# Kernel tuning notes

Measured on AMD Instinct MI355X. Metric: run time of the kernel, lower is better.

## Reference

```python
import jax, jax.numpy as jnp
import numpy as np

NEG_INF = -9e15  # matches the torch module's zero_vec constant
ALPHA = 0.2      # LeakyReLU negative slope


def setup_inputs() -> dict:
    key = jax.random.key(0)
    k1, k2, k3, k4, k5, k6 = jax.random.split(key, 6)
    N_t, N_o, F_in, F_out = 8192, 8192, 256, 64
    return {
        "t_input": jax.random.normal(k1, (N_t, F_in), dtype=jnp.float32),
        "o_input": jax.random.normal(k2, (N_o, F_in), dtype=jnp.float32),
        "W_t": jax.random.normal(k3, (F_in, F_out), dtype=jnp.float32) * 0.1,
        "W_o": jax.random.normal(k4, (F_in, F_out), dtype=jnp.float32) * 0.1,
        "a": jax.random.normal(k5, (2 * F_out, 1), dtype=jnp.float32) * 0.1,
        "adj": jax.random.randint(k6, (N_t, N_o), 0, 2, dtype=jnp.int32),
    }


def reference(t_input, o_input, W_t, W_o, a, adj):
    # Linear projections
    h_t = t_input @ W_t            # [N_t, F]
    h_o = o_input @ W_o            # [N_o, F]
    F_out = h_t.shape[1]
    a_t = a[:F_out, 0]             # [F]
    a_o = a[F_out:, 0]             # [F]
    # e[i,j] = leakyrelu(cat(h_t[i], h_o[j]) . a) = leakyrelu(h_t[i].a_t + h_o[j].a_o)
    # (avoids materializing the N_t*N_o*2F concat tensor; same math)
    e = jax.nn.leaky_relu(
        (h_t @ a_t)[:, None] + (h_o @ a_o)[None, :], negative_slope=ALPHA
    )                              # [N_t, N_o]
    attention = jnp.where(adj > 0, e, NEG_INF)
    attention = jax.nn.softmax(attention, axis=1)
    # dropout is identity at eval time
    h_prime = attention @ h_o      # [N_t, F]
    return jax.nn.elu(h_prime)     # concat=True
```

## Files before the change

### kernel.cpp

```cpp
#include <hip/hip_runtime.h>
#include <math.h>

#define NT 8192
#define NO 8192
#define FIN 256
#define FOUT 64
#define SPLIT 8
#define JSP (NO/SPLIT)
#define ROWT 64

#define OFF_ST  ((size_t)0)
#define OFF_SO  (OFF_ST + (size_t)NT)
#define OFF_WT  (OFF_SO + (size_t)NO)
#define OFF_WO  (OFF_WT + (size_t)FIN)
#define OFF_NUM (OFF_WO + (size_t)FIN)
#define OFF_DEN (OFF_NUM + (size_t)SPLIT*NT*FOUT)
#define OFF_HOB (OFF_DEN + (size_t)SPLIT*NT)
#define OFF_ETA (OFF_HOB + (size_t)NO*FOUT/2)

typedef __attribute__((ext_vector_type(8))) short short8;
typedef __attribute__((ext_vector_type(4))) float float4v;

static __device__ __forceinline__ unsigned short f2bf(float x) {
  unsigned int u = __float_as_uint(x);
  unsigned int r = (u + 0x7fffu + ((u >> 16) & 1u)) >> 16;
  return (unsigned short)r;
}
static __device__ __forceinline__ int pk2(float a, float b) {
  return (int)((unsigned int)f2bf(a) | ((unsigned int)f2bf(b) << 16));
}
static __device__ __forceinline__ float bflo(int p) {
  return __uint_as_float(((unsigned int)p) << 16);
}
static __device__ __forceinline__ float bfhi(int p) {
  return __uint_as_float(((unsigned int)p) & 0xffff0000u);
}

__global__ void k_wvec(const float* __restrict__ Wt, const float* __restrict__ Wo,
                       const float* __restrict__ a, float* __restrict__ ws) {
  int k = threadIdx.x;
  float s1 = 0.f, s2 = 0.f;
#pragma unroll
  for (int fq = 0; fq < FOUT/4; ++fq) {
    float4 wt4 = *(const float4*)(Wt + (size_t)k*FOUT + fq*4);
    float4 wo4 = *(const float4*)(Wo + (size_t)k*FOUT + fq*4);
    float4 at4 = *(const float4*)(a + fq*4);
    float4 ao4 = *(const float4*)(a + FOUT + fq*4);
    s1 += wt4.x*at4.x + wt4.y*at4.y + wt4.z*at4.z + wt4.w*at4.w;
    s2 += wo4.x*ao4.x + wo4.y*ao4.y + wo4.z*ao4.z + wo4.w*ao4.w;
  }
  ws[OFF_WT + k] = s1;
  ws[OFF_WO + k] = s2;
}

__global__ void k_st(const float* __restrict__ tin, float* __restrict__ ws) {
  int lane = threadIdx.x & 63;
  int wv   = threadIdx.x >> 6;
  int row  = blockIdx.x * 4 + wv;
  float4 v = ((const float4*)(tin + (size_t)row*FIN))[lane];
  float4 w = ((const float4*)(ws + OFF_WT))[lane];
  float p = v.x*w.x + v.y*w.y + v.z*w.z + v.w*w.w;
#pragma unroll
  for (int m = 32; m >= 1; m >>= 1) p += __shfl_xor(p, m, 64);
  if (lane == 0) ws[OFF_ST + row] = p;
}

__global__ void k_ho(const float* __restrict__ oin, const float* __restrict__ Wo,
                     const float* __restrict__ a, float* __restrict__ ws) {
  unsigned short* hobp = (unsigned short*)(ws + OFF_HOB);
  int lane = threadIdx.x & 63;
  int wv = __builtin_amdgcn_readfirstlane(threadIdx.x >> 6);
  int r0 = blockIdx.x * 16 + wv * 4;
  const float* ob = oin + (size_t)r0 * FIN;
  float acc[4];
#pragma unroll
  for (int r = 0; r < 4; ++r) acc[r] = 0.f;
#pragma unroll 2
  for (int k = 0; k < FIN; k += 4) {
    float w0 = Wo[(size_t)(k+0)*FOUT + lane];
    float w1 = Wo[(size_t)(k+1)*FOUT + lane];
    float w2 = Wo[(size_t)(k+2)*FOUT + lane];
    float w3 = Wo[(size_t)(k+3)*FOUT + lane];
#pragma unroll
    for (int r = 0; r < 4; ++r) {
      float4 ov = *(const float4*)(ob + (size_t)r*FIN + k);
      acc[r] = fmaf(ov.x, w0, acc[r]);
      acc[r] = fmaf(ov.y, w1, acc[r]);
      acc[r] = fmaf(ov.z, w2, acc[r]);
      acc[r] = fmaf(ov.w, w3, acc[r]);
    }
  }
  float ao = a[FOUT + lane];
  int fg = lane >> 4, n16 = lane & 15;
#pragma unroll
  for (int r = 0; r < 4; ++r) {
    int j = r0 + r;
    int jt = j >> 5, jl = j & 31;
    int ldst = (jl >> 3) * 16 + n16;
    int e = jl & 7;
    hobp[(((size_t)jt*4 + fg)*64 + ldst)*8 + e] = f2bf(acc[r]);
    float p = acc[r] * ao;
#pragma unroll
    for (int m = 32; m >= 1; m >>= 1) p += __shfl_xor(p, m, 64);
    if (lane == 0) ws[OFF_SO + j] = p;
  }
}

__global__ void k_etab(float* __restrict__ ws) {
  int j = blockIdx.x * 256 + threadIdx.x;
  float s = ws[OFF_SO + j];
  ws[OFF_ETA + 2*j + 0] = __expf(s);
  ws[OFF_ETA + 2*j + 1] = __expf(0.2f * s);
}

__launch_bounds__(256, 4)
__global__ void k_attn(const int* __restrict__ adj, float* __restrict__ ws) {
  const float* st = ws + OFF_ST;
  const float* etab = ws + OFF_ETA;
  const unsigned short* hobp = (const unsigned short*)(ws + OFF_HOB);
  float* gnum = ws + OFF_NUM;
  float* gden = ws + OFF_DEN;

  int t = threadIdx.x;
  int wv = t >> 6, lane = t & 63;
  int bx = blockIdx.x;
  int s  = bx & (SPLIT - 1);
  int bi = bx >> 3;
  int i0 = bi * ROWT;
  int jb = s * JSP;

  int rsrc = lane >> 2, csrc = lane & 3;
  int irow_s = i0 + wv*16 + rsrc;
  float sti  = st[irow_s];
  float esti  = __expf(sti);
  float esti2 = __expf(0.2f * sti);
  float ethr  = __expf(-sti);

  const int* arow = adj + (size_t)irow_s * NO + jb + csrc*8;
  const float* ep = etab + (size_t)(jb + csrc*8) * 2;
  const unsigned short* hpb = hobp + (size_t)(jb >> 5) * 2048 + lane*8;

  int r16 = lane & 15, kg = lane >> 4;
  int sidx4 = ((r16 * 4 + kg) << 2);

  float4v acc0 = (float4v)0.f, acc1 = (float4v)0.f;
  float4v acc2 = (float4v)0.f, acc3 = (float4v)0.f;
  float dsum = 0.f;

  int4 a0 = *(const int4*)(arow);
  int4 a1 = *(const int4*)(arow + 4);

#pragma unroll 1
  for (int tt = 0; tt < JSP/32; ++tt) {
    int ttn = (tt < JSP/32 - 1) ? tt + 1 : tt;
    int4 n0 = *(const int4*)(arow + ttn*32);
    int4 n1 = *(const int4*)(arow + ttn*32 + 4);

    const float* e_ = ep + tt*64;
    float4 e0 = *(const float4*)(e_);
    float4 e1 = *(const float4*)(e_ + 4);
    float4 e2 = *(const float4*)(e_ + 8);
    float4 e3 = *(const float4*)(e_ + 12);
    const unsigned short* hb = hpb + (size_t)tt*2048;
    short8 b0 = *(const short8*)(hb);
    short8 b1 = *(const short8*)(hb + 512);
    short8 b2 = *(const short8*)(hb + 1024);
    short8 b3 = *(const short8*)(hb + 1536);

    float w0 = ((e0.x >= ethr) ? esti*e0.x : esti2*e0.y); w0 = (a0.x > 0) ? w0 : 0.f;
    float w1 = ((e0.z >= ethr) ? esti*e0.z : esti2*e0.w); w1 = (a0.y > 0) ? w1 : 0.f;
    float w2 = ((e1.x >= ethr) ? esti*e1.x : esti2*e1.y); w2 = (a0.z > 0) ? w2 : 0.f;
    float w3 = ((e1.z >= ethr) ? esti*e1.z : esti2*e1.w); w3 = (a0.w > 0) ? w3 : 0.f;
    float w4 = ((e2.x >= ethr) ? esti*e2.x : esti2*e2.y); w4 = (a1.x > 0) ? w4 : 0.f;
    float w5 = ((e2.z >= ethr) ? esti*e2.z : esti2*e2.w); w5 = (a1.y > 0) ? w5 : 0.f;
    float w6 = ((e3.x >= ethr) ? esti*e3.x : esti2*e3.y); w6 = (a1.z > 0) ? w6 : 0.f;
    float w7 = ((e3.z >= ethr) ? esti*e3.z : esti2*e3.w); w7 = (a1.w > 0) ? w7 : 0.f;

    int p0 = pk2(w0, w1);
    int p1 = pk2(w2, w3);
    int p2 = pk2(w4, w5);
    int p3 = pk2(w6, w7);
    dsum += bflo(p0) + bfhi(p0) + bflo(p1) + bfhi(p1)
          + bflo(p2) + bfhi(p2) + bflo(p3) + bfhi(p3);

    int4 ai;
    ai.x = __builtin_amdgcn_ds_bpermute(sidx4, p0);
    ai.y = __builtin_amdgcn_ds_bpermute(sidx4, p1);
    ai.z = __builtin_amdgcn_ds_bpermute(sidx4, p2);
    ai.w = __builtin_amdgcn_ds_bpermute(sidx4, p3);
    short8 afrag = *(short8*)&ai;

    acc0 = __builtin_amdgcn_mfma_f32_16x16x32_bf16(afrag, b0, acc0, 0, 0, 0);
    acc1 = __builtin_amdgcn_mfma_f32_16x16x32_bf16(afrag, b1, acc1, 0, 0, 0);
    acc2 = __builtin_amdgcn_mfma_f32_16x16x32_bf16(afrag, b2, acc2, 0, 0, 0);
    acc3 = __builtin_amdgcn_mfma_f32_16x16x32_bf16(afrag, b3, acc3, 0, 0, 0);

    a0 = n0; a1 = n1;
  }

  dsum += __shfl_xor(dsum, 1, 64);
  dsum += __shfl_xor(dsum, 2, 64);
  if (csrc == 0) gden[(size_t)s*NT + i0 + wv*16 + rsrc] = dsum;

  size_t obase = ((size_t)s*NT + i0 + wv*16 + kg*4) * FOUT + r16;
#pragma unroll
  for (int r = 0; r < 4; ++r) {
    gnum[obase + (size_t)r*FOUT +  0] = acc0[r];
    gnum[obase + (size_t)r*FOUT + 16] = acc1[r];
    gnum[obase + (size_t)r*FOUT + 32] = acc2[r];
    gnum[obase + (size_t)r*FOUT + 48] = acc3[r];
  }
}

__global__ void k_comb(const float* __restrict__ ws, float* __restrict__ out) {
  int idx = blockIdx.x * 256 + threadIdx.x;
  int i = idx >> 6;
  float num = 0.f, den = 0.f;
#pragma unroll
  for (int s = 0; s < SPLIT; ++s) {
    num += ws[OFF_NUM + ((size_t)s*NT + i)*FOUT + (idx & 63)];
    den += ws[OFF_DEN + (size_t)s*NT + i];
  }
  float r = num / den;
  out[idx] = (r > 0.f) ? r : (__expf(r) - 1.f);
}

extern "C" void kernel_launch(void* const* d_in, const int* in_sizes, int n_in,
                              void* d_out, int out_size, void* d_ws, size_t ws_size,
                              hipStream_t stream) {
  const float* tin = (const float*)d_in[0];
  const float* oin = (const float*)d_in[1];
  const float* Wt  = (const float*)d_in[2];
  const float* Wo  = (const float*)d_in[3];
  const float* a   = (const float*)d_in[4];
  const int*   adj = (const int*)d_in[5];
  float* out = (float*)d_out;
  float* ws  = (float*)d_ws;

  hipLaunchKernelGGL(k_wvec, dim3(1),              dim3(256), 0, stream, Wt, Wo, a, ws);
  hipLaunchKernelGGL(k_st,   dim3(NT/4),           dim3(256), 0, stream, tin, ws);
  hipLaunchKernelGGL(k_ho,   dim3(NO/16),          dim3(256), 0, stream, oin, Wo, a, ws);
  hipLaunchKernelGGL(k_etab, dim3(NO/256),         dim3(256), 0, stream, ws);
  hipLaunchKernelGGL(k_attn, dim3(NT/ROWT*SPLIT),  dim3(256), 0, stream, adj, ws);
  hipLaunchKernelGGL(k_comb, dim3(NT*FOUT/256),    dim3(256), 0, stream, ws, out);
}
```

Measured before the change: 449.6 us.

## Fuse small prep kernels, deepen adj prefetch with nontemporal loads

Folds the W_t·a_t vector computation into k_st, where each block recomputes it into shared memory and then handles 64 rows. The exp table is now written directly from k_ho, which drops the k_wvec and k_etab launches. In the attention loop, adj is prefetched two tiles ahead using nontemporal loads and the loop is manually unrolled by two. This cuts launch overhead and is meant to hide more adj streaming latency, at the cost of redundant per-block weight-vector work and extra registers.

```diff
diff --git a/kernel.cpp b/kernel.cpp
--- a/kernel.cpp
+++ b/kernel.cpp
@@ -20,6 +20,7 @@
 
 typedef __attribute__((ext_vector_type(8))) short short8;
 typedef __attribute__((ext_vector_type(4))) float float4v;
+typedef __attribute__((ext_vector_type(4))) int int4v;
 
 static __device__ __forceinline__ unsigned short f2bf(float x) {
   unsigned int u = __float_as_uint(x);
@@ -35,34 +36,36 @@
 static __device__ __forceinline__ float bfhi(int p) {
   return __uint_as_float(((unsigned int)p) & 0xffff0000u);
 }
-
-__global__ void k_wvec(const float* __restrict__ Wt, const float* __restrict__ Wo,
-                       const float* __restrict__ a, float* __restrict__ ws) {
+static __device__ __forceinline__ int4v ntld(const int* p) {
+  return __builtin_nontemporal_load((const int4v*)p);
+}
+
+__global__ void k_st(const float* __restrict__ tin, const float* __restrict__ Wt,
+                     const float* __restrict__ a, float* __restrict__ ws) {
+  __shared__ float wt_s[FIN];
   int k = threadIdx.x;
-  float s1 = 0.f, s2 = 0.f;
+  float s1 = 0.f;
 #pragma unroll
   for (int fq = 0; fq < FOUT/4; ++fq) {
     float4 wt4 = *(const float4*)(Wt + (size_t)k*FOUT + fq*4);
-    float4 wo4 = *(const float4*)(Wo + (size_t)k*FOUT + fq*4);
     float4 at4 = *(const float4*)(a + fq*4);
-    float4 ao4 = *(const float4*)(a + FOUT + fq*4);
     s1 += wt4.x*at4.x + wt4.y*at4.y + wt4.z*at4.z + wt4.w*at4.w;
-    s2 += wo4.x*ao4.x + wo4.y*ao4.y + wo4.z*ao4.z + wo4.w*ao4.w;
-  }
-  ws[OFF_WT + k] = s1;
-  ws[OFF_WO + k] = s2;
-}
-
-__global__ void k_st(const float* __restrict__ tin, float* __restrict__ ws) {
+  }
+  wt_s[k] = s1;
+  __syncthreads();
+
   int lane = threadIdx.x & 63;
   int wv   = threadIdx.x >> 6;
-  int row  = blockIdx.x * 4 + wv;
-  float4 v = ((const float4*)(tin + (size_t)row*FIN))[lane];
-  float4 w = ((const float4*)(ws + OFF_WT))[lane];
-  float p = v.x*w.x + v.y*w.y + v.z*w.z + v.w*w.w;
-#pragma unroll
-  for (int m = 32; m >= 1; m >>= 1) p += __shfl_xor(p, m, 64);
-  if (lane == 0) ws[OFF_ST + row] = p;
+  float4 w = ((const float4*)wt_s)[lane];
+#pragma unroll
+  for (int r = 0; r < 16; ++r) {
+    int row = blockIdx.x * 64 + wv * 16 + r;
+    float4 v = ((const float4*)(tin + (size_t)row*FIN))[lane];
+    float p = v.x*w.x + v.y*w.y + v.z*w.z + v.w*w.w;
+#pragma unroll
+    for (int m = 32; m >= 1; m >>= 1) p += __shfl_xor(p, m, 64);
+    if (lane == 0) ws[OFF_ST + row] = p;
+  }
 }
 
 __global__ void k_ho(const float* __restrict__ oin, const float* __restrict__ Wo,
@@ -102,16 +105,49 @@
     float p = acc[r] * ao;
 #pragma unroll
     for (int m = 32; m >= 1; m >>= 1) p += __shfl_xor(p, m, 64);
-    if (lane == 0) ws[OFF_SO + j] = p;
-  }
-}
-
-__global__ void k_etab(float* __restrict__ ws) {
-  int j = blockIdx.x * 256 + threadIdx.x;
-  float s = ws[OFF_SO + j];
-  ws[OFF_ETA + 2*j + 0] = __expf(s);
-  ws[OFF_ETA + 2*j + 1] = __expf(0.2f * s);
-}
+    if (lane == 0) {
+      ws[OFF_ETA + 2*j + 0] = __expf(p);
+      ws[OFF_ETA + 2*j + 1] = __expf(0.2f * p);
+    }
+  }
+}
+
+#define ATTN_BODY(TT, A0, A1) do {                                             \
+    const float* e_ = ep + (TT)*64;                                            \
+    float4 e0 = *(const float4*)(e_);                                          \
+    float4 e1 = *(const float4*)(e_ + 4);                                      \
+    float4 e2 = *(const float4*)(e_ + 8);                                      \
+    float4 e3 = *(const float4*)(e_ + 12);                                     \
+    const unsigned short* hb = hpb + (size_t)(TT)*2048;                        \
+    short8 b0 = *(const short8*)(hb);                                          \
+    short8 b1 = *(const short8*)(hb + 512);                                    \
+    short8 b2 = *(const short8*)(hb + 1024);                                   \
+    short8 b3 = *(const short8*)(hb + 1536);                                   \
+    float w0 = ((e0.x >= ethr) ? esti*e0.x : esti2*e0.y); w0 = ((A0).x > 0) ? w0 : 0.f; \
+    float w1 = ((e0.z >= ethr) ? esti*e0.z : esti2*e0.w); w1 = ((A0).y > 0) ? w1 : 0.f; \
+    float w2 = ((e1.x >= ethr) ? esti*e1.x : esti2*e1.y); w2 = ((A0).z > 0) ? w2 : 0.f; \
+    float w3 = ((e1.z >= ethr) ? esti*e1.z : esti2*e1.w); w3 = ((A0).w > 0) ? w3 : 0.f; \
+    float w4 = ((e2.x >= ethr) ? esti*e2.x : esti2*e2.y); w4 = ((A1).x > 0) ? w4 : 0.f; \
+    float w5 = ((e2.z >= ethr) ? esti*e2.z : esti2*e2.w); w5 = ((A1).y > 0) ? w5 : 0.f; \
+    float w6 = ((e3.x >= ethr) ? esti*e3.x : esti2*e3.y); w6 = ((A1).z > 0) ? w6 : 0.f; \
+    float w7 = ((e3.z >= ethr) ? esti*e3.z : esti2*e3.w); w7 = ((A1).w > 0) ? w7 : 0.f; \
+    int p0 = pk2(w0, w1);                                                      \
+    int p1 = pk2(w2, w3);                                                      \
+    int p2 = pk2(w4, w5);                                                      \
+    int p3 = pk2(w6, w7);                                                      \
+    dsum += bflo(p0) + bfhi(p0) + bflo(p1) + bfhi(p1)                          \
+          + bflo(p2) + bfhi(p2) + bflo(p3) + bfhi(p3);                         \
+    int4 ai;                                                                   \
+    ai.x = __builtin_amdgcn_ds_bpermute(sidx4, p0);                            \
+    ai.y = __builtin_amdgcn_ds_bpermute(sidx4, p1);                            \
+    ai.z = __builtin_amdgcn_ds_bpermute(sidx4, p2);                            \
+    ai.w = __builtin_amdgcn_ds_bpermute(sidx4, p3);                            \
+    short8 afrag = *(short8*)&ai;                                              \
+    acc0 = __builtin_amdgcn_mfma_f32_16x16x32_bf16(afrag, b0, acc0, 0, 0, 0);  \
+    acc1 = __builtin_amdgcn_mfma_f32_16x16x32_bf16(afrag, b1, acc1, 0, 0, 0);  \
+    acc2 = __builtin_amdgcn_mfma_f32_16x16x32_bf16(afrag, b2, acc2, 0, 0, 0);  \
+    acc3 = __builtin_amdgcn_mfma_f32_16x16x32_bf16(afrag, b3, acc3, 0, 0, 0);  \
+  } while (0)
 
 __launch_bounds__(256, 4)
 __global__ void k_attn(const int* __restrict__ adj, float* __restrict__ ws) {
@@ -147,55 +183,21 @@
   float4v acc2 = (float4v)0.f, acc3 = (float4v)0.f;
   float dsum = 0.f;
 
-  int4 a0 = *(const int4*)(arow);
-  int4 a1 = *(const int4*)(arow + 4);
+  const int NTT = JSP/32;
+  int4v c0a = ntld(arow);           int4v c1a = ntld(arow + 4);
+  int4v c0b = ntld(arow + 32);      int4v c1b = ntld(arow + 36);
 
 #pragma unroll 1
-  for (int tt = 0; tt < JSP/32; ++tt) {
-    int ttn = (tt < JSP/32 - 1) ? tt + 1 : tt;
-    int4 n0 = *(const int4*)(arow + ttn*32);
-    int4 n1 = *(const int4*)(arow + ttn*32 + 4);
-
-    const float* e_ = ep + tt*64;
-    float4 e0 = *(const float4*)(e_);
-    float4 e1 = *(const float4*)(e_ + 4);
-    float4 e2 = *(const float4*)(e_ + 8);
-    float4 e3 = *(const float4*)(e_ + 12);
-    const unsigned short* hb = hpb + (size_t)tt*2048;
-    short8 b0 = *(const short8*)(hb);
-    short8 b1 = *(const short8*)(hb + 512);
-    short8 b2 = *(const short8*)(hb + 1024);
-    short8 b3 = *(const short8*)(hb + 1536);
-
-    float w0 = ((e0.x >= ethr) ? esti*e0.x : esti2*e0.y); w0 = (a0.x > 0) ? w0 : 0.f;
-    float w1 = ((e0.z >= ethr) ? esti*e0.z : esti2*e0.w); w1 = (a0.y > 0) ? w1 : 0.f;
-    float w2 = ((e1.x >= ethr) ? esti*e1.x : esti2*e1.y); w2 = (a0.z > 0) ? w2 : 0.f;
-    float w3 = ((e1.z >= ethr) ? esti*e1.z : esti2*e1.w); w3 = (a0.w > 0) ? w3 : 0.f;
-    float w4 = ((e2.x >= ethr) ? esti*e2.x : esti2*e2.y); w4 = (a1.x > 0) ? w4 : 0.f;
-    float w5 = ((e2.z >= ethr) ? esti*e2.z : esti2*e2.w); w5 = (a1.y > 0) ? w5 : 0.f;
-    float w6 = ((e3.x >= ethr) ? esti*e3.x : esti2*e3.y); w6 = (a1.z > 0) ? w6 : 0.f;
-    float w7 = ((e3.z >= ethr) ? esti*e3.z : esti2*e3.w); w7 = (a1.w > 0) ? w7 : 0.f;
-
-    int p0 = pk2(w0, w1);
-    int p1 = pk2(w2, w3);
-    int p2 = pk2(w4, w5);
-    int p3 = pk2(w6, w7);
-    dsum += bflo(p0) + bfhi(p0) + bflo(p1) + bfhi(p1)
-          + bflo(p2) + bfhi(p2) + bflo(p3) + bfhi(p3);
-
-    int4 ai;
-    ai.x = __builtin_amdgcn_ds_bpermute(sidx4, p0);
-    ai.y = __builtin_amdgcn_ds_bpermute(sidx4, p1);
-    ai.z = __builtin_amdgcn_ds_bpermute(sidx4, p2);
-    ai.w = __builtin_amdgcn_ds_bpermute(sidx4, p3);
-    short8 afrag = *(short8*)&ai;
-
-    acc0 = __builtin_amdgcn_mfma_f32_16x16x32_bf16(afrag, b0, acc0, 0, 0, 0);
-    acc1 = __builtin_amdgcn_mfma_f32_16x16x32_bf16(afrag, b1, acc1, 0, 0, 0);
-    acc2 = __builtin_amdgcn_mfma_f32_16x16x32_bf16(afrag, b2, acc2, 0, 0, 0);
-    acc3 = __builtin_amdgcn_mfma_f32_16x16x32_bf16(afrag, b3, acc3, 0, 0, 0);
-
-    a0 = n0; a1 = n1;
+  for (int tt = 0; tt < NTT; tt += 2) {
+    int t2 = (tt + 2 < NTT) ? tt + 2 : tt;
+    int4v n0a = ntld(arow + t2*32);
+    int4v n1a = ntld(arow + t2*32 + 4);
+    ATTN_BODY(tt, c0a, c1a);
+    int t3 = (tt + 3 < NTT) ? tt + 3 : tt + 1;
+    int4v n0b = ntld(arow + t3*32);
+    int4v n1b = ntld(arow + t3*32 + 4);
+    ATTN_BODY(tt + 1, c0b, c1b);
+    c0a = n0a; c1a = n1a; c0b = n0b; c1b = n1b;
   }
 
   dsum += __shfl_xor(dsum, 1, 64);
@@ -237,10 +239,8 @@
   float* out = (float*)d_out;
   float* ws  = (float*)d_ws;
 
-  hipLaunchKernelGGL(k_wvec, dim3(1),              dim3(256), 0, stream, Wt, Wo, a, ws);
-  hipLaunchKernelGGL(k_st,   dim3(NT/4),           dim3(256), 0, stream, tin, ws);
+  hipLaunchKernelGGL(k_st,   dim3(NT/64),          dim3(256), 0, stream, tin, Wt, a, ws);
   hipLaunchKernelGGL(k_ho,   dim3(NO/16),          dim3(256), 0, stream, oin, Wo, a, ws);
-  hipLaunchKernelGGL(k_etab, dim3(NO/256),         dim3(256), 0, stream, ws);
   hipLaunchKernelGGL(k_attn, dim3(NT/ROWT*SPLIT),  dim3(256), 0, stream, adj, ws);
   hipLaunchKernelGGL(k_comb, dim3(NT*FOUT/256),    dim3(256), 0, stream, ws, out);
 }
```

Measured after the change: 448.9 us. About the same (-0.2%).
